# Kernel tuning notes

Hardware: AMD Instinct MI355X
Metric: run time of the kernel (lower is better)

## Reference

```python
import jax, jax.numpy as jnp
import numpy as np

D_CONV = 4
D_STATE = 32
DT_RANK = 16


def setup_inputs() -> dict:
    key = jax.random.key(0)
    ks = jax.random.split(key, 12)
    B, D, L, DI = 4, 256, 1024, 256
    s = 0.02
    return {
        "x": jax.random.normal(ks[0], (B, D, L), jnp.float32),
        "Win": jax.random.normal(ks[1], (4, D, 2 * DI), jnp.float32) * s,
        "Wconv": jax.random.normal(ks[2], (4, DI, D_CONV), jnp.float32) * 0.2,
        "bconv": jnp.zeros((4, DI), jnp.float32),
        "Wxp": jax.random.normal(ks[3], (4, DI, DT_RANK + 2 * D_STATE), jnp.float32) * s,
        "Wdt": jax.random.normal(ks[4], (4, DT_RANK, DI), jnp.float32) * s,
        "bdt": jnp.full((4, DI), -2.0, jnp.float32),
        "Alog": jnp.tile(jnp.log(jnp.arange(1, D_STATE + 1, dtype=jnp.float32))[None, None, :], (4, DI, 1)),
        "Dskip": jnp.ones((4, DI), jnp.float32),
        "Wout": jax.random.normal(ks[5], (4, DI, D), jnp.float32) * s,
        "Wg": jax.random.normal(ks[6], (2, L, L), jnp.float32) * 0.01,
        "bg": jnp.zeros((2, L), jnp.float32),
        "alpha": jnp.ones((2,), jnp.float32),
        "gamma": jnp.ones((2, L), jnp.float32),
        "beta": jnp.zeros((2, L), jnp.float32),
    }


def _selective_scan(u, dt, Bm, Cm, A):
    # u, dt: [B,L,di]; Bm, Cm: [B,L,N]; A: [di,N]
    dBu = dt * u
    def step(h, inp):
        dt_t, dbu_t, B_t, C_t = inp  # [B,di],[B,di],[B,N],[B,N]
        h = jnp.exp(dt_t[:, :, None] * A) * h + dbu_t[:, :, None] * B_t[:, None, :]
        y = jnp.einsum('bdn,bn->bd', h, C_t)
        return h, y
    xs = (jnp.moveaxis(dt, 1, 0), jnp.moveaxis(dBu, 1, 0),
          jnp.moveaxis(Bm, 1, 0), jnp.moveaxis(Cm, 1, 0))
    h0 = jnp.zeros((u.shape[0], A.shape[0], A.shape[1]), u.dtype)
    _, ys = jax.lax.scan(step, h0, xs)  # ys: [L,B,di]
    return jnp.moveaxis(ys, 0, 1)


def _mamba_layer(x_bdl, Win, Wconv, bconv, Wxp, Wdt, bdt, Alog, Dskip, Wout):
    x = jnp.swapaxes(x_bdl, 1, 2)  # [B,L,D]
    L = x.shape[1]
    u, z = jnp.split(x @ Win, 2, axis=-1)  # each [B,L,di]
    up = jnp.pad(u, ((0, 0), (D_CONV - 1, 0), (0, 0)))
    u = sum(up[:, k:k + L, :] * Wconv[:, k] for k in range(D_CONV)) + bconv
    u = jax.nn.silu(u)
    proj = u @ Wxp
    dtp = proj[..., :DT_RANK]
    Bm = proj[..., DT_RANK:DT_RANK + D_STATE]
    Cm = proj[..., DT_RANK + D_STATE:]
    dt = jax.nn.softplus(dtp @ Wdt + bdt)
    y = _selective_scan(u, dt, Bm, Cm, -jnp.exp(Alog)) + u * Dskip
    y = y * jax.nn.silu(z)
    return jnp.swapaxes(y @ Wout, 1, 2)  # [B,d_out,L]


def _forward(x, Win, Wconv, bconv, Wxp, Wdt, bdt, Alog, Dskip, Wout, Wg, bg, alpha, gamma, beta):
    def branch(inp, i0, i1, j):
        h = _mamba_layer(inp, Win[i0], Wconv[i0], bconv[i0], Wxp[i0], Wdt[i0], bdt[i0], Alog[i0], Dskip[i0], Wout[i0])
        h = _mamba_layer(h, Win[i1], Wconv[i1], bconv[i1], Wxp[i1], Wdt[i1], bdt[i1], Alog[i1], Dskip[i1], Wout[i1])
        return gamma[j] * jnp.tanh(alpha[j] * h) + beta[j]  # DyTanh over last dim
    def gate(j):
        return jax.nn.sigmoid(jnp.einsum('bdl,ml->bdm', x, Wg[j]) + bg[j])
    m = branch(x, 0, 1, 0) * gate(0)
    rx = jnp.flip(x, axis=-1)
    rm = branch(rx, 2, 3, 1) * gate(1)
    return m + jnp.flip(rm, axis=-1)


def reference(x, Win, Wconv, bconv, Wxp, Wdt, bdt, Alog, Dskip, Wout, Wg, bg, alpha, gamma, beta):
    return _forward(x, Win, Wconv, bconv, Wxp, Wdt, bdt, Alog, Dskip, Wout, Wg, bg, alpha, gamma, beta)
```

## Files before the change

kernel.cpp:

```cpp
#include <hip/hip_runtime.h>


#define LSEQ 1024
#define SCAN_CL 16
#define SCAN_NC 64

#if __has_builtin(__builtin_amdgcn_exp2f)
#define EXP2(x) __builtin_amdgcn_exp2f(x)
#else
#define EXP2(x) exp2f(x)
#endif

typedef short bf16x8 __attribute__((ext_vector_type(8)));
typedef float f32x4 __attribute__((ext_vector_type(4)));

__device__ __forceinline__ float sigmoidf_(float x) { return 1.f / (1.f + __expf(-x)); }
__device__ __forceinline__ float siluf_(float x)    { return x / (1.f + __expf(-x)); }
__device__ __forceinline__ float softplusf_(float x){ return x > 20.f ? x : log1pf(__expf(x)); }

__device__ __forceinline__ unsigned short bf16rne_(float v) {
  unsigned u = __float_as_uint(v);
  return (unsigned short)((u + 0x7FFFu + ((u >> 16) & 1u)) >> 16);
}
__device__ __forceinline__ float bfto_(unsigned short h) {
  return __uint_as_float(((unsigned)h) << 16);
}
__device__ __forceinline__ void split3_(float v, unsigned short& h,
                                        unsigned short& m, unsigned short& l) {
  h = bf16rne_(v); float r = v - bfto_(h);
  m = bf16rne_(r); float r2 = r - bfto_(m);
  l = bf16rne_(r2);
}

__device__ __forceinline__ long swzi(long idx, long row) {
  return idx ^ (((row >> 1) & 3) << 3);
}

__device__ void tconv3_body(const float* __restrict__ in,
                            unsigned short* __restrict__ oh,
                            unsigned short* __restrict__ om,
                            unsigned short* __restrict__ ol,
                            int K, int N, int bx, int by, int z) {
  __shared__ float T[32][33];
  int n0 = bx * 32, k0 = by * 32;
  int tx = threadIdx.x & 31, ty = threadIdx.x >> 5;
  const float* src = in + (long)z * K * N;
#pragma unroll
  for (int m = 0; m < 4; ++m)
    T[ty + 8 * m][tx] = src[(long)(k0 + ty + 8 * m) * N + n0 + tx];
  __syncthreads();
  long obase = (long)z * N * K;
#pragma unroll
  for (int m = 0; m < 4; ++m) {
    float v = T[tx][ty + 8 * m];
    int n = n0 + ty + 8 * m;
    long o = swzi(obase + (long)n * K + k0 + tx, n);
    split3_(v, oh[o], om[o], ol[o]);
  }
}

__device__ void split3v_body(const float4* __restrict__ in,
                             unsigned short* __restrict__ oh,
                             unsigned short* __restrict__ om,
                             unsigned short* __restrict__ ol, int i) {
  float4 v = in[i];
  long b = 4L * i;
  long sb = swzi(b, b >> 10);
  ushort4 H, M, L;
  split3_(v.x, H.x, M.x, L.x); split3_(v.y, H.y, M.y, L.y);
  split3_(v.z, H.z, M.z, L.z); split3_(v.w, H.w, M.w, L.w);
  *(ushort4*)(oh + sb) = H; *(ushort4*)(om + sb) = M; *(ushort4*)(ol + sb) = L;
}

__global__ __launch_bounds__(256)
void preprocess_kernel(const float* __restrict__ x, const float* __restrict__ Wg,
                       const float* __restrict__ Win, const float* __restrict__ Wout,
                       const float* __restrict__ Alog,
                       unsigned short* __restrict__ Xh, unsigned short* __restrict__ Xm,
                       unsigned short* __restrict__ Xl,
                       unsigned short* __restrict__ XGh, unsigned short* __restrict__ XGm,
                       unsigned short* __restrict__ XGl,
                       unsigned short* __restrict__ Wgh, unsigned short* __restrict__ Wgm,
                       unsigned short* __restrict__ Wgl,
                       unsigned short* __restrict__ WinTh, unsigned short* __restrict__ WinTm,
                       unsigned short* __restrict__ WinTl,
                       unsigned short* __restrict__ WoutTh, unsigned short* __restrict__ WoutTm,
                       unsigned short* __restrict__ WoutTl,
                       float* __restrict__ Aneg) {
  const int bid = blockIdx.x;
  if (bid < 8192) {
    long idx = (long)bid * 256 + threadIdx.x;
    int d = (int)(idx & 255);
    long t = idx >> 8;
    int l = (int)(t & 1023);
    int t2 = (int)(t >> 10);
    int b = t2 & 3;
    int j = t2 >> 2;
    int lsrc = j ? (1023 - l) : l;
    float v = x[((long)(b * 256 + d)) * LSEQ + lsrc];
    long o = swzi(idx, t);
    split3_(v, Xh[o], Xm[o], Xl[o]);
  } else if (bid < 9216) {
    int i = (bid - 8192) * 256 + threadIdx.x;
    split3v_body((const float4*)x, XGh, XGm, XGl, i);
  } else if (bid < 11264) {
    int i = (bid - 9216) * 256 + threadIdx.x;
    split3v_body((const float4*)Wg, Wgh, Wgm, Wgl, i);
  } else if (bid < 11776) {
    int t = bid - 11264;
    tconv3_body(Win, WinTh, WinTm, WinTl, 256, 512, t & 15, (t >> 4) & 7, t >> 7);
  } else if (bid < 12032) {
    int t = bid - 11776;
    tconv3_body(Wout, WoutTh, WoutTm, WoutTl, 256, 256, t & 7, (t >> 3) & 7, t >> 6);
  } else {
    int idx = (bid - 12032) * 256 + threadIdx.x;
    Aneg[idx] = -__expf(Alog[idx]) * 1.4426950408889634f;
  }
}

__device__ __forceinline__ void gload16(const unsigned short* g, unsigned short* l) {
  __builtin_amdgcn_global_load_lds(
      (const __attribute__((address_space(1))) unsigned int*)g,
      (__attribute__((address_space(3))) unsigned int*)l, 16, 0, 0);
}

template <int KSPLIT>
__global__ __launch_bounds__(256)
void gemm_mfma(const unsigned short* __restrict__ Ah_g,
               const unsigned short* __restrict__ Am_g,
               const unsigned short* __restrict__ Al_g, long aZ, int lda,
               const unsigned short* __restrict__ Bh_g,
               const unsigned short* __restrict__ Bm_g,
               const unsigned short* __restrict__ Bl_g, long bZ, int ldb,
               float* __restrict__ C, long cZ, int N, int KH) {
  __shared__ unsigned short S[6][128 * 32];
  const int bz = blockIdx.z;
  const int z  = (KSPLIT == 2) ? (bz >> 1) : bz;
  const int kh = (KSPLIT == 2) ? (bz & 1) : 0;
  const int m0 = blockIdx.y * 128, n0 = blockIdx.x * 128;
  const int tid = threadIdx.x;

  const long khoff = (long)kh * KH;
  const long a0 = (long)z * aZ + (long)(m0 + (tid >> 2)) * lda + khoff + (tid & 3) * 8;
  const long a1 = a0 + 64L * lda;
  const long b0 = (long)z * bZ + (long)(n0 + (tid >> 2)) * ldb + khoff + (tid & 3) * 8;
  const long b1 = b0 + 64L * ldb;
  const int l0 = tid * 8, l1 = tid * 8 + 2048;

  const int lane = tid & 63, w = tid >> 6;
  const int wr = w >> 1, wc = w & 1;
  const int fr = lane & 15, g = lane >> 4;

  f32x4 acc[4][4];
#pragma unroll
  for (int i = 0; i < 4; ++i)
#pragma unroll
    for (int j = 0; j < 4; ++j)
#pragma unroll
      for (int q = 0; q < 4; ++q) acc[i][j][q] = 0.f;

  for (int k0 = 0; k0 < KH; k0 += 32) {
    __syncthreads();
    gload16(Ah_g + a0 + k0, &S[0][l0]); gload16(Ah_g + a1 + k0, &S[0][l1]);
    gload16(Am_g + a0 + k0, &S[1][l0]); gload16(Am_g + a1 + k0, &S[1][l1]);
    gload16(Al_g + a0 + k0, &S[2][l0]); gload16(Al_g + a1 + k0, &S[2][l1]);
    gload16(Bh_g + b0 + k0, &S[3][l0]); gload16(Bh_g + b1 + k0, &S[3][l1]);
    gload16(Bm_g + b0 + k0, &S[4][l0]); gload16(Bm_g + b1 + k0, &S[4][l1]);
    gload16(Bl_g + b0 + k0, &S[5][l0]); gload16(Bl_g + b1 + k0, &S[5][l1]);
    __syncthreads();

    bf16x8 fb[3][4];
#pragma unroll
    for (int nf = 0; nf < 4; ++nf) {
      int rb = wc * 64 + nf * 16 + fr;
      int ob = rb * 32 + ((g ^ ((rb >> 1) & 3)) << 3);
      fb[0][nf] = *(const bf16x8*)&S[3][ob];
      fb[1][nf] = *(const bf16x8*)&S[4][ob];
      fb[2][nf] = *(const bf16x8*)&S[5][ob];
    }
#pragma unroll
    for (int mf = 0; mf < 4; ++mf) {
      int ra = wr * 64 + mf * 16 + fr;
      int oa = ra * 32 + ((g ^ ((ra >> 1) & 3)) << 3);
      bf16x8 fah = *(const bf16x8*)&S[0][oa];
      bf16x8 fam = *(const bf16x8*)&S[1][oa];
      bf16x8 fal = *(const bf16x8*)&S[2][oa];
#pragma unroll
      for (int nf = 0; nf < 4; ++nf) {
        acc[mf][nf] = __builtin_amdgcn_mfma_f32_16x16x32_bf16(fah, fb[0][nf], acc[mf][nf], 0, 0, 0);
        acc[mf][nf] = __builtin_amdgcn_mfma_f32_16x16x32_bf16(fah, fb[1][nf], acc[mf][nf], 0, 0, 0);
        acc[mf][nf] = __builtin_amdgcn_mfma_f32_16x16x32_bf16(fam, fb[0][nf], acc[mf][nf], 0, 0, 0);
        acc[mf][nf] = __builtin_amdgcn_mfma_f32_16x16x32_bf16(fam, fb[1][nf], acc[mf][nf], 0, 0, 0);
        acc[mf][nf] = __builtin_amdgcn_mfma_f32_16x16x32_bf16(fah, fb[2][nf], acc[mf][nf], 0, 0, 0);
        acc[mf][nf] = __builtin_amdgcn_mfma_f32_16x16x32_bf16(fal, fb[0][nf], acc[mf][nf], 0, 0, 0);
      }
    }
  }

  float* Cz = C + (long)bz * cZ;
#pragma unroll
  for (int mf = 0; mf < 4; ++mf)
#pragma unroll
    for (int nf = 0; nf < 4; ++nf) {
      int col = n0 + wc * 64 + nf * 16 + fr;
      int row0 = m0 + wr * 64 + mf * 16 + g * 4;
#pragma unroll
      for (int q = 0; q < 4; ++q)
        Cz[(long)(row0 + q) * N + col] = acc[mf][nf][q];
    }
}

template <int OP>
__global__ __launch_bounds__(256)
void combine2_kernel(const float* __restrict__ P, long pz,
                     const float* __restrict__ bias, int nmask,
                     float* __restrict__ outF,
                     unsigned short* __restrict__ oh,
                     unsigned short* __restrict__ om,
                     unsigned short* __restrict__ ol, long oz) {
  int z = blockIdx.y;
  long i = (long)blockIdx.x * 256 + threadIdx.x;
  float v = P[(long)(2 * z) * pz + i] + P[(long)(2 * z + 1) * pz + i];
  if (OP == 1) {
    outF[(long)z * oz + i] = sigmoidf_(v + bias[z * (nmask + 1) + (int)(i & nmask)]);
  } else if (OP == 0) {
    outF[(long)z * oz + i] = v;
  } else {
    long o = (long)z * oz + swzi(i, i >> 8);
    split3_(v, oh[o], om[o], ol[o]);
  }
}

__global__ __launch_bounds__(256)
void gemm23_kernel(const float* __restrict__ UC, const float* __restrict__ Wxp,
                   const float* __restrict__ Wdt, const float* __restrict__ bdt,
                   float* __restrict__ PROJ, float* __restrict__ DTo, int stage) {
  __shared__ float As[16][17];
  __shared__ float Ws[16][80];
  __shared__ float PR[16][17];
  __shared__ float WD[16][256];
  const int z = blockIdx.y;
  const int lidx = stage + 2 * z;
  const int m0 = blockIdx.x * 16;
  const long abase = (long)z * 4096 * 256 + (long)m0 * 256;
  const float* W = Wxp + (long)lidx * 256 * 80;
  const int tid = threadIdx.x;
  const int tx = tid & 15, ty = tid >> 4;

#pragma unroll
  for (int t = 0; t < 16; ++t) {
    int e = t * 256 + tid;
    WD[e >> 8][e & 255] = Wdt[(long)lidx * 4096 + e];
  }

  float acc[5];
#pragma unroll
  for (int j = 0; j < 5; ++j) acc[j] = 0.f;

  for (int k0 = 0; k0 < 256; k0 += 16) {
    {
      As[tx][ty] = UC[abase + (long)ty * 256 + k0 + tx];
    }
    {
      int k = tid >> 4, cg2 = (tid & 15) * 5;
#pragma unroll
      for (int i2 = 0; i2 < 5; ++i2)
        Ws[k][cg2 + i2] = W[(long)(k0 + k) * 80 + cg2 + i2];
    }
    __syncthreads();
#pragma unroll
    for (int kk = 0; kk < 16; ++kk) {
      float a = As[kk][ty];
#pragma unroll
      for (int j = 0; j < 5; ++j)
        acc[j] = fmaf(a, Ws[kk][tx * 5 + j], acc[j]);
    }
    __syncthreads();
  }

#pragma unroll
  for (int j = 0; j < 5; ++j) {
    int c = tx * 5 + j;
    float v = acc[j];
    PROJ[((long)z * 4096 + m0 + ty) * 80 + c] = v;
    if (c < 16) PR[ty][c] = v;
  }
  __syncthreads();

  for (int it = 0; it < 16; ++it) {
    float ssum = 0.f;
#pragma unroll
    for (int k = 0; k < 16; ++k) ssum = fmaf(PR[it][k], WD[k][tid], ssum);
    DTo[((long)z * 4096 + m0 + it) * 256 + tid] =
        softplusf_(ssum + bdt[lidx * 256 + tid]);
  }
}

__global__ __launch_bounds__(256) void conv_kernel(const float* __restrict__ UZ,
                                                   const float* __restrict__ Wconv,
                                                   const float* __restrict__ bconv,
                                                   float* __restrict__ uc, int stage) {
  long idx = (long)blockIdx.x * 256 + threadIdx.x;
  int di = (int)(idx & 255);
  long r = idx >> 8;
  int l = (int)(r & 1023);
  int j = (int)(r >> 12);
  int lidx = stage + 2 * j;
  const float* wc = Wconv + (long)(lidx * 256 + di) * 4;
  float acc = bconv[lidx * 256 + di];
  const float* up = UZ + (r - 3) * 512 + di;
  if (l >= 3) {
    acc = fmaf(up[0], wc[0], acc);
    acc = fmaf(up[512], wc[1], acc);
    acc = fmaf(up[1024], wc[2], acc);
    acc = fmaf(up[1536], wc[3], acc);
  } else {
    for (int k = 3 - l; k < 4; ++k) acc = fmaf(up[(long)k * 512], wc[k], acc);
  }
  uc[idx] = acc * sigmoidf_(acc);
}

template <int PASS>
__global__ __launch_bounds__(256)
void scan_chunk_kernel(const float* __restrict__ dt,
                       const float* __restrict__ uc,
                       const float* __restrict__ UZ,
                       const float* __restrict__ proj,
                       const float* __restrict__ Aneg,
                       const float* __restrict__ Dskip,
                       float* __restrict__ HST,
                       float* __restrict__ DTS,
                       unsigned short* __restrict__ YGh,
                       unsigned short* __restrict__ YGm,
                       unsigned short* __restrict__ YGl, int stage) {
  __shared__ __align__(16) float BC[SCAN_CL][64];
  const int blk = blockIdx.x;
  const int chunk = blk & (SCAN_NC - 1);
  const int jb = blk >> 6;
  const int di = threadIdx.x;
  const int j = jb >> 2;
  const int lidx = stage + 2 * j;
  const long r0 = (long)jb * 1024 + (long)chunk * SCAN_CL;

  for (int e = threadIdx.x; e < SCAN_CL * 64; e += 256) {
    int l = e >> 6, col = e & 63;
    BC[l][col] = proj[(r0 + l) * 80 + 16 + col];
  }

  float A[32];
  {
    const float4* ap = (const float4*)(Aneg + ((long)(lidx * 256 + di)) * 32);
#pragma unroll
    for (int q = 0; q < 8; ++q) {
      float4 v = ap[q];
      A[4 * q] = v.x; A[4 * q + 1] = v.y; A[4 * q + 2] = v.z; A[4 * q + 3] = v.w;
    }
  }

  const long sbase = (((long)jb * SCAN_NC + chunk) * 256 + di) * 32;
  float h[32];
  if (PASS == 0) {
#pragma unroll
    for (int n = 0; n < 32; ++n) h[n] = 0.f;
  } else {
    const float4* hp = (const float4*)(HST + sbase);
#pragma unroll
    for (int q = 0; q < 8; ++q) {
      float4 v = hp[q];
      h[4 * q] = v.x; h[4 * q + 1] = v.y; h[4 * q + 2] = v.z; h[4 * q + 3] = v.w;
    }
  }

  float Dsk = 0.f, dtsum = 0.f;
  if (PASS == 1) Dsk = Dskip[lidx * 256 + di];

  const float* dtp = dt + r0 * 256 + di;
  const float* up  = uc + r0 * 256 + di;
  const float* zp  = UZ + r0 * 512 + 256 + di;

  __syncthreads();

  float Db[2][8], Ub[2][8], Zb[2][8];
#pragma unroll
  for (int i = 0; i < 8; ++i) {
    Db[0][i] = dtp[(long)i * 256];
    Ub[0][i] = up[(long)i * 256];
    if (PASS == 1) Zb[0][i] = zp[(long)i * 512];
  }

#pragma unroll
  for (int bt = 0; bt < SCAN_CL / 8; ++bt) {
    const int cur = bt & 1, nxt = cur ^ 1;
    if (bt < SCAN_CL / 8 - 1) {
#pragma unroll
      for (int i = 0; i < 8; ++i) {
        long l = (long)(bt + 1) * 8 + i;
        Db[nxt][i] = dtp[l * 256];
        Ub[nxt][i] = up[l * 256];
        if (PASS == 1) Zb[nxt][i] = zp[l * 512];
      }
    }
#pragma unroll
    for (int i = 0; i < 8; ++i) {
      const int l = bt * 8 + i;
      float dtv = Db[cur][i];
      float uv  = Ub[cur][i];
      float du  = dtv * uv;
      if (PASS == 0) dtsum += dtv;
      float yacc[4] = {0.f, 0.f, 0.f, 0.f};
      const float4* bc4 = (const float4*)&BC[l][0];
#pragma unroll
      for (int q = 0; q < 8; ++q) {
        float4 bv = bc4[q];
        float4 cv = bc4[8 + q];
        const float* bp = &bv.x;
        const float* cp = &cv.x;
#pragma unroll
        for (int k = 0; k < 4; ++k) {
          int n = 4 * q + k;
          float a = EXP2(dtv * A[n]);
          h[n] = fmaf(a, h[n], du * bp[k]);
          yacc[n & 3] = fmaf(h[n], cp[k], yacc[n & 3]);
        }
      }
      if (PASS == 1) {
        float y = (yacc[0] + yacc[1]) + (yacc[2] + yacc[3]);
        float zv = Zb[cur][i];
        float val = (y + uv * Dsk) * siluf_(zv);
        long o = swzi((r0 + l) * 256 + di, r0 + l);
        split3_(val, YGh[o], YGm[o], YGl[o]);
      }
    }
  }

  if (PASS == 0) {
    float4* hp = (float4*)(HST + sbase);
#pragma unroll
    for (int q = 0; q < 8; ++q)
      hp[q] = make_float4(h[4 * q], h[4 * q + 1], h[4 * q + 2], h[4 * q + 3]);
    DTS[((long)jb * SCAN_NC + chunk) * 256 + di] = dtsum;
  }
}

__global__ __launch_bounds__(256)
void scan_combine_kernel(float* __restrict__ HST, const float* __restrict__ DTS,
                         const float* __restrict__ Aneg, int stage) {
  int t = blockIdx.x * 256 + threadIdx.x;
  int n = t & 31;
  int di = (t >> 5) & 255;
  int jb = t >> 13;
  int lidx = stage + 2 * (jb >> 2);
  float A = Aneg[((long)(lidx * 256 + di)) * 32 + n];
  float hs = 0.f;
  for (int cb = 0; cb < SCAN_NC; cb += 8) {
    float s[8], P[8], hv[8];
#pragma unroll
    for (int i = 0; i < 8; ++i) {
      long base = ((long)jb * SCAN_NC + cb + i) * 256 + di;
      s[i] = HST[base * 32 + n];
      P[i] = DTS[base];
    }
#pragma unroll
    for (int i = 0; i < 8; ++i) P[i] = EXP2(A * P[i]);
#pragma unroll
    for (int i = 0; i < 8; ++i) {
      hv[i] = hs;
      hs = fmaf(P[i], hs, s[i]);
    }
#pragma unroll
    for (int i = 0; i < 8; ++i) {
      long base = ((long)jb * SCAN_NC + cb + i) * 256 + di;
      HST[base * 32 + n] = hv[i];
    }
  }
}

__global__ __launch_bounds__(256) void combine_kernel(const float* __restrict__ H,
                                                      const float* __restrict__ gate,
                                                      const float* __restrict__ alpha,
                                                      const float* __restrict__ gamma,
                                                      const float* __restrict__ beta,
                                                      float* __restrict__ out) {
  long idx = (long)blockIdx.x * 256 + threadIdx.x;
  int l = (int)(idx & 1023);
  long t = idx >> 10;
  int d = (int)(t & 255);
  int b = (int)(t >> 8);
  int lr = 1023 - l;
  float h0 = H[(((long)b * 1024 + l) * 256) + d];
  float h1 = H[(((long)(4 + b) * 1024 + lr) * 256) + d];
  float g0 = gate[((long)(b * 256 + d)) * 1024 + l];
  float g1 = gate[(long)1024 * 1024 + ((long)(b * 256 + d)) * 1024 + lr];
  float m0 = (gamma[l] * tanhf(alpha[0] * h0) + beta[l]) * g0;
  float m1 = (gamma[1024 + lr] * tanhf(alpha[1] * h1) + beta[1024 + lr]) * g1;
  out[idx] = m0 + m1;
}

extern "C" void kernel_launch(void* const* d_in, const int* in_sizes, int n_in,
                              void* d_out, int out_size, void* d_ws, size_t ws_size,
                              hipStream_t stream) {
  const float* x     = (const float*)d_in[0];
  const float* Win   = (const float*)d_in[1];
  const float* Wconv = (const float*)d_in[2];
  const float* bconv = (const float*)d_in[3];
  const float* Wxp   = (const float*)d_in[4];
  const float* Wdt   = (const float*)d_in[5];
  const float* bdt   = (const float*)d_in[6];
  const float* Alog  = (const float*)d_in[7];
  const float* Dskip = (const float*)d_in[8];
  const float* Wout  = (const float*)d_in[9];
  const float* Wg    = (const float*)d_in[10];
  const float* bg    = (const float*)d_in[11];
  const float* alpha = (const float*)d_in[12];
  const float* gamma = (const float*)d_in[13];
  const float* beta  = (const float*)d_in[14];
  float* out = (float*)d_out;

  float* ws   = (float*)d_ws;
  float* UZ   = ws;
  float* UC   = UZ + 4194304;
  float* PROJ = UC + 2097152;
  float* DT   = PROJ + 655360;
  float* GATE = DT + 2097152;
  float* ANEG = GATE + 2097152;
  float* HST  = ANEG + 32768;
  float* DTS  = HST + 4194304;
  float* XF   = DTS + 131072;
  float* PG   = XF + 2097152;
  unsigned short* Xpl  = (unsigned short*)(PG + 4194304);
  unsigned short* YGpl = Xpl + 3 * 2097152;
  unsigned short* XGpl = YGpl + 3 * 2097152;
  unsigned short* Wgpl = XGpl + 3 * 1048576;
  unsigned short* WinT = Wgpl + 3 * 2097152;
  unsigned short* WoutT = WinT + 3 * 524288;
  unsigned short* Xh = Xpl, *Xm = Xpl + 2097152, *Xl = Xpl + 2 * 2097152;
  unsigned short* YGh = YGpl, *YGm = YGpl + 2097152, *YGl = YGpl + 2 * 2097152;
  unsigned short* XGh = XGpl, *XGm = XGpl + 1048576, *XGl = XGpl + 2 * 1048576;
  unsigned short* Wgh = Wgpl, *Wgm = Wgpl + 2097152, *Wgl = Wgpl + 2 * 2097152;
  unsigned short* WinTh = WinT, *WinTm = WinT + 524288, *WinTl = WinT + 2 * 524288;
  unsigned short* WoutTh = WoutT, *WoutTm = WoutT + 262144, *WoutTl = WoutT + 2 * 262144;

  preprocess_kernel<<<dim3(12160), dim3(256), 0, stream>>>(
      x, Wg, Win, Wout, Alog, Xh, Xm, Xl, XGh, XGm, XGl,
      Wgh, Wgm, Wgl, WinTh, WinTm, WinTl, WoutTh, WoutTm, WoutTl, ANEG);

  gemm_mfma<2><<<dim3(8, 8, 4), dim3(256), 0, stream>>>(
      XGh, XGm, XGl, 0L, 1024,
      Wgh, Wgm, Wgl, (long)1024 * 1024, 1024,
      PG, (long)1024 * 1024, 1024, 512);
  combine2_kernel<1><<<dim3(4096, 2), dim3(256), 0, stream>>>(
      PG, (long)1024 * 1024, bg, 1023, GATE, nullptr, nullptr, nullptr,
      (long)1024 * 1024);

  for (int s = 0; s < 2; ++s) {
    gemm_mfma<1><<<dim3(4, 32, 2), dim3(256), 0, stream>>>(
        Xh, Xm, Xl, (long)4096 * 256, 256,
        WinTh + (long)s * 131072, WinTm + (long)s * 131072, WinTl + (long)s * 131072,
        (long)262144, 256,
        UZ, (long)4096 * 512, 512, 256);

    conv_kernel<<<dim3(8192), dim3(256), 0, stream>>>(UZ, Wconv, bconv, UC, s);

    gemm23_kernel<<<dim3(256, 2), dim3(256), 0, stream>>>(
        UC, Wxp, Wdt, bdt, PROJ, DT, s);

    scan_chunk_kernel<0><<<dim3(8 * SCAN_NC), dim3(256), 0, stream>>>(
        DT, UC, UZ, PROJ, ANEG, Dskip, HST, DTS, YGh, YGm, YGl, s);
    scan_combine_kernel<<<dim3(256), dim3(256), 0, stream>>>(HST, DTS, ANEG, s);
    scan_chunk_kernel<1><<<dim3(8 * SCAN_NC), dim3(256), 0, stream>>>(
        DT, UC, UZ, PROJ, ANEG, Dskip, HST, DTS, YGh, YGm, YGl, s);

    gemm_mfma<2><<<dim3(2, 32, 4), dim3(256), 0, stream>>>(
        YGh, YGm, YGl, (long)4096 * 256, 256,
        WoutTh + (long)s * 65536, WoutTm + (long)s * 65536, WoutTl + (long)s * 65536,
        (long)131072, 256,
        PG, (long)4096 * 256, 256, 128);
    if (s == 0) {
      combine2_kernel<2><<<dim3(4096, 2), dim3(256), 0, stream>>>(
          PG, (long)4096 * 256, nullptr, 0, nullptr, Xh, Xm, Xl, (long)4096 * 256);
    } else {
      combine2_kernel<0><<<dim3(4096, 2), dim3(256), 0, stream>>>(
          PG, (long)4096 * 256, nullptr, 0, XF, nullptr, nullptr, nullptr,
          (long)4096 * 256);
    }
  }

  combine_kernel<<<dim3(4096), dim3(256), 0, stream>>>(XF, GATE, alpha, gamma, beta, out);
}
```

Baseline: 331.3 us.

## Add split-K to gate and input projection GEMMs, fuse partial sums into consumers

The gate GEMM now splits K four ways, doubling its grid so more workgroups run at once. The input projection GEMM gains a two-way split-K, and its two partial planes are summed inside the conv and scan kernels rather than in a separate reduction pass. The goal is better occupancy on small-grid GEMMs. The cost is extra partial-sum memory traffic and extra loads in the conv and scan kernels, plus a larger workspace.

```diff
diff --git a/kernel.cpp b/kernel.cpp
--- a/kernel.cpp
+++ b/kernel.cpp
@@ -4,6 +4,7 @@
 #define LSEQ 1024
 #define SCAN_CL 16
 #define SCAN_NC 64
+#define G1PLANE 2097152L
 
 #if __has_builtin(__builtin_amdgcn_exp2f)
 #define EXP2(x) __builtin_amdgcn_exp2f(x)
@@ -135,8 +136,8 @@
                float* __restrict__ C, long cZ, int N, int KH) {
   __shared__ unsigned short S[6][128 * 32];
   const int bz = blockIdx.z;
-  const int z  = (KSPLIT == 2) ? (bz >> 1) : bz;
-  const int kh = (KSPLIT == 2) ? (bz & 1) : 0;
+  const int z  = bz / KSPLIT;
+  const int kh = bz % KSPLIT;
   const int m0 = blockIdx.y * 128, n0 = blockIdx.x * 128;
   const int tid = threadIdx.x;
 
@@ -210,9 +211,9 @@
     }
 }
 
-template <int OP>
+template <int OP, int NP>
 __global__ __launch_bounds__(256)
-void combine2_kernel(const float* __restrict__ P, long pz,
+void combineN_kernel(const float* __restrict__ P, long pz,
                      const float* __restrict__ bias, int nmask,
                      float* __restrict__ outF,
                      unsigned short* __restrict__ oh,
@@ -220,7 +221,9 @@
                      unsigned short* __restrict__ ol, long oz) {
   int z = blockIdx.y;
   long i = (long)blockIdx.x * 256 + threadIdx.x;
-  float v = P[(long)(2 * z) * pz + i] + P[(long)(2 * z + 1) * pz + i];
+  float v = 0.f;
+#pragma unroll
+  for (int p = 0; p < NP; ++p) v += P[(long)(z * NP + p) * pz + i];
   if (OP == 1) {
     outF[(long)z * oz + i] = sigmoidf_(v + bias[z * (nmask + 1) + (int)(i & nmask)]);
   } else if (OP == 0) {
@@ -258,9 +261,7 @@
   for (int j = 0; j < 5; ++j) acc[j] = 0.f;
 
   for (int k0 = 0; k0 < 256; k0 += 16) {
-    {
-      As[tx][ty] = UC[abase + (long)ty * 256 + k0 + tx];
-    }
+    As[tx][ty] = UC[abase + (long)ty * 256 + k0 + tx];
     {
       int k = tid >> 4, cg2 = (tid & 15) * 5;
 #pragma unroll
@@ -296,7 +297,7 @@
   }
 }
 
-__global__ __launch_bounds__(256) void conv_kernel(const float* __restrict__ UZ,
+__global__ __launch_bounds__(256) void conv_kernel(const float* __restrict__ PG1,
                                                    const float* __restrict__ Wconv,
                                                    const float* __restrict__ bconv,
                                                    float* __restrict__ uc, int stage) {
@@ -308,14 +309,17 @@
   int lidx = stage + 2 * j;
   const float* wc = Wconv + (long)(lidx * 256 + di) * 4;
   float acc = bconv[lidx * 256 + di];
-  const float* up = UZ + (r - 3) * 512 + di;
+  long rr = r & 4095;
+  const float* u0 = PG1 + (long)(j * 2) * G1PLANE + (rr - 3) * 512 + di;
+  const float* u1 = u0 + G1PLANE;
   if (l >= 3) {
-    acc = fmaf(up[0], wc[0], acc);
-    acc = fmaf(up[512], wc[1], acc);
-    acc = fmaf(up[1024], wc[2], acc);
-    acc = fmaf(up[1536], wc[3], acc);
+    acc = fmaf(u0[0]    + u1[0],    wc[0], acc);
+    acc = fmaf(u0[512]  + u1[512],  wc[1], acc);
+    acc = fmaf(u0[1024] + u1[1024], wc[2], acc);
+    acc = fmaf(u0[1536] + u1[1536], wc[3], acc);
   } else {
-    for (int k = 3 - l; k < 4; ++k) acc = fmaf(up[(long)k * 512], wc[k], acc);
+    for (int k = 3 - l; k < 4; ++k)
+      acc = fmaf(u0[(long)k * 512] + u1[(long)k * 512], wc[k], acc);
   }
   uc[idx] = acc * sigmoidf_(acc);
 }
@@ -324,7 +328,7 @@
 __global__ __launch_bounds__(256)
 void scan_chunk_kernel(const float* __restrict__ dt,
                        const float* __restrict__ uc,
-                       const float* __restrict__ UZ,
+                       const float* __restrict__ PG1,
                        const float* __restrict__ proj,
                        const float* __restrict__ Aneg,
                        const float* __restrict__ Dskip,
@@ -376,7 +380,8 @@
 
   const float* dtp = dt + r0 * 256 + di;
   const float* up  = uc + r0 * 256 + di;
-  const float* zp  = UZ + r0 * 512 + 256 + di;
+  const float* zp0 = PG1 + (long)(j * 2) * G1PLANE + (r0 & 4095) * 512 + 256 + di;
+  const float* zp1 = zp0 + G1PLANE;
 
   __syncthreads();
 
@@ -385,7 +390,7 @@
   for (int i = 0; i < 8; ++i) {
     Db[0][i] = dtp[(long)i * 256];
     Ub[0][i] = up[(long)i * 256];
-    if (PASS == 1) Zb[0][i] = zp[(long)i * 512];
+    if (PASS == 1) Zb[0][i] = zp0[(long)i * 512] + zp1[(long)i * 512];
   }
 
 #pragma unroll
@@ -397,7 +402,7 @@
         long l = (long)(bt + 1) * 8 + i;
         Db[nxt][i] = dtp[l * 256];
         Ub[nxt][i] = up[l * 256];
-        if (PASS == 1) Zb[nxt][i] = zp[l * 512];
+        if (PASS == 1) Zb[nxt][i] = zp0[l * 512] + zp1[l * 512];
       }
     }
 #pragma unroll
@@ -517,8 +522,7 @@
   float* out = (float*)d_out;
 
   float* ws   = (float*)d_ws;
-  float* UZ   = ws;
-  float* UC   = UZ + 4194304;
+  float* UC   = ws;
   float* PROJ = UC + 2097152;
   float* DT   = PROJ + 655360;
   float* GATE = DT + 2097152;
@@ -527,7 +531,7 @@
   float* DTS  = HST + 4194304;
   float* XF   = DTS + 131072;
   float* PG   = XF + 2097152;
-  unsigned short* Xpl  = (unsigned short*)(PG + 4194304);
+  unsigned short* Xpl  = (unsigned short*)(PG + 8388608);
   unsigned short* YGpl = Xpl + 3 * 2097152;
   unsigned short* XGpl = YGpl + 3 * 2097152;
   unsigned short* Wgpl = XGpl + 3 * 1048576;
@@ -544,31 +548,31 @@
       x, Wg, Win, Wout, Alog, Xh, Xm, Xl, XGh, XGm, XGl,
       Wgh, Wgm, Wgl, WinTh, WinTm, WinTl, WoutTh, WoutTm, WoutTl, ANEG);
 
-  gemm_mfma<2><<<dim3(8, 8, 4), dim3(256), 0, stream>>>(
+  gemm_mfma<4><<<dim3(8, 8, 8), dim3(256), 0, stream>>>(
       XGh, XGm, XGl, 0L, 1024,
       Wgh, Wgm, Wgl, (long)1024 * 1024, 1024,
-      PG, (long)1024 * 1024, 1024, 512);
-  combine2_kernel<1><<<dim3(4096, 2), dim3(256), 0, stream>>>(
+      PG, (long)1024 * 1024, 1024, 256);
+  combineN_kernel<1, 4><<<dim3(4096, 2), dim3(256), 0, stream>>>(
       PG, (long)1024 * 1024, bg, 1023, GATE, nullptr, nullptr, nullptr,
       (long)1024 * 1024);
 
   for (int s = 0; s < 2; ++s) {
-    gemm_mfma<1><<<dim3(4, 32, 2), dim3(256), 0, stream>>>(
+    gemm_mfma<2><<<dim3(4, 32, 4), dim3(256), 0, stream>>>(
         Xh, Xm, Xl, (long)4096 * 256, 256,
         WinTh + (long)s * 131072, WinTm + (long)s * 131072, WinTl + (long)s * 131072,
         (long)262144, 256,
-        UZ, (long)4096 * 512, 512, 256);
-
-    conv_kernel<<<dim3(8192), dim3(256), 0, stream>>>(UZ, Wconv, bconv, UC, s);
+        PG, G1PLANE, 512, 128);
+
+    conv_kernel<<<dim3(8192), dim3(256), 0, stream>>>(PG, Wconv, bconv, UC, s);
 
     gemm23_kernel<<<dim3(256, 2), dim3(256), 0, stream>>>(
         UC, Wxp, Wdt, bdt, PROJ, DT, s);
 
     scan_chunk_kernel<0><<<dim3(8 * SCAN_NC), dim3(256), 0, stream>>>(
-        DT, UC, UZ, PROJ, ANEG, Dskip, HST, DTS, YGh, YGm, YGl, s);
+        DT, UC, PG, PROJ, ANEG, Dskip, HST, DTS, YGh, YGm, YGl, s);
     scan_combine_kernel<<<dim3(256), dim3(256), 0, stream>>>(HST, DTS, ANEG, s);
     scan_chunk_kernel<1><<<dim3(8 * SCAN_NC), dim3(256), 0, stream>>>(
-        DT, UC, UZ, PROJ, ANEG, Dskip, HST, DTS, YGh, YGm, YGl, s);
+        DT, UC, PG, PROJ, ANEG, Dskip, HST, DTS, YGh, YGm, YGl, s);
 
     gemm_mfma<2><<<dim3(2, 32, 4), dim3(256), 0, stream>>>(
         YGh, YGm, YGl, (long)4096 * 256, 256,
@@ -576,10 +580,10 @@
         (long)131072, 256,
         PG, (long)4096 * 256, 256, 128);
     if (s == 0) {
-      combine2_kernel<2><<<dim3(4096, 2), dim3(256), 0, stream>>>(
+      combineN_kernel<2, 2><<<dim3(4096, 2), dim3(256), 0, stream>>>(
           PG, (long)4096 * 256, nullptr, 0, nullptr, Xh, Xm, Xl, (long)4096 * 256);
     } else {
-      combine2_kernel<0><<<dim3(4096, 2), dim3(256), 0, stream>>>(
+      combineN_kernel<0, 2><<<dim3(4096, 2), dim3(256), 0, stream>>>(
           PG, (long)4096 * 256, nullptr, 0, XF, nullptr, nullptr, nullptr,
           (long)4096 * 256);
     }
```

After: 337.0 us. About the same (+1.7%).
